# Optimization experiments

Measured on AMD Instinct MI355X. Metric: run time of the kernel, lower is better.

Reference implementation:

```python
import jax, jax.numpy as jnp
import numpy as np

FEATURE_DIM = 128
NUM_EDGES = 640000
NUM_NODES = 40000


def setup_inputs() -> dict:
    key = jax.random.key(0)
    ks = jax.random.split(key, 10)
    d = FEATURE_DIM
    scale = 1.0 / np.sqrt(d)
    inp = {
        "messages": jax.random.normal(ks[0], (NUM_EDGES, d), dtype=jnp.float32),
        "receivers": jax.random.randint(ks[1], (NUM_EDGES,), 0, NUM_NODES, dtype=jnp.int32),
        "num_segments": NUM_NODES,
        "Wk": jax.random.normal(ks[2], (d, d), dtype=jnp.float32) * scale,
        "bk": jnp.zeros((d,), dtype=jnp.float32),
        "Wv": jax.random.normal(ks[3], (d, d), dtype=jnp.float32) * scale,
        "bv": jnp.zeros((d,), dtype=jnp.float32),
        "Wq": jax.random.normal(ks[4], (d, d), dtype=jnp.float32) * scale,
        "bq": jnp.zeros((d,), dtype=jnp.float32),
        "Wo": jax.random.normal(ks[5], (d, d), dtype=jnp.float32) * scale,
        "bo": jnp.zeros((d,), dtype=jnp.float32),
    }
    return inp


def reference(messages, receivers, num_segments, Wk, bk, Wv, bv, Wq, bq, Wo, bo):
    d = messages.shape[-1]
    # per-edge key/value projections
    keys = messages @ Wk + bk            # [E, d]
    values = messages @ Wv + bv          # [E, d]
    # node-level summed messages -> queries
    summed = jax.ops.segment_sum(messages, receivers, num_segments)  # [N, d]
    queries = summed @ Wq + bq                                       # [N, d]
    # scalar attention score per edge (dot over full feature dim)
    msg_q = queries[receivers]                                       # [E, d]
    scores = jnp.sum(msg_q * keys, axis=-1) / jnp.sqrt(jnp.float32(d))  # [E]
    # segment softmax over edges sharing a receiver
    max_s = jax.ops.segment_max(scores, receivers, num_segments)     # [N]
    exp_s = jnp.exp(scores - max_s[receivers])                       # [E]
    sum_e = jax.ops.segment_sum(exp_s, receivers, num_segments)      # [N]
    attn = exp_s / (sum_e[receivers] + 1e-08)                        # [E]
    # weighted scatter-sum of values, then output projection
    agg = jax.ops.segment_sum(values * attn[:, None], receivers, num_segments)  # [N, d]
    return agg @ Wo + bo
```

## Files before the change

kernel.cpp:

```cpp
#include <hip/hip_runtime.h>

#define D 128
#define RSQRT_D 0.088388347648318440550f
#define NEG_HUGE -3.4e38f
#define NPB 8
#define CAP 288
#define DTHR 20.0f

#define FMA4(acc, s, b) { acc.x += (s)*(b).x; acc.y += (s)*(b).y; acc.z += (s)*(b).z; acc.w += (s)*(b).w; }
#define ADD4(acc, b) { acc.x += (b).x; acc.y += (b).y; acc.z += (b).z; acc.w += (b).w; }
#define MRG4(a) { a.x += __shfl_xor(a.x,32); a.y += __shfl_xor(a.y,32); a.z += __shfl_xor(a.z,32); a.w += __shfl_xor(a.w,32); }
#define SCL4(a, f) { a.x *= (f); a.y *= (f); a.z *= (f); a.w *= (f); }
#define Z4 make_float4(0.f,0.f,0.f,0.f)

#define MERGE_HALVES(mi, si, ci) { \
    float mo_ = __shfl_xor(mi, 32); \
    float so_ = __shfl_xor(si, 32); \
    float4 co_; co_.x = __shfl_xor(ci.x, 32); co_.y = __shfl_xor(ci.y, 32); \
    co_.z = __shfl_xor(ci.z, 32); co_.w = __shfl_xor(ci.w, 32); \
    float mt_ = fmaxf(mi, mo_); \
    float e0_ = __expf(mi - mt_), e1_ = __expf(mo_ - mt_); \
    si = si * e0_ + so_ * e1_; \
    ci.x = ci.x * e0_ + co_.x * e1_; ci.y = ci.y * e0_ + co_.y * e1_; \
    ci.z = ci.z * e0_ + co_.z * e1_; ci.w = ci.w * e0_ + co_.w * e1_; \
}

__global__ __launch_bounds__(256) void prep_kernel(
    const float* __restrict__ Wq, const float* __restrict__ Wk,
    const float* __restrict__ bq, const float* __restrict__ bk,
    const float* __restrict__ Wv, const float* __restrict__ Wo,
    const float* __restrict__ bv,
    float* __restrict__ Wqk, float* __restrict__ bqk,
    float* __restrict__ wqb, float* __restrict__ bqb,
    float* __restrict__ Wvo, float* __restrict__ bvo,
    int* __restrict__ zbase, int zcount) {
    int bid = blockIdx.x, t = threadIdx.x;
    if (bid < 64) {
        int i = bid * 2 + (t >> 7), j = t & 127;
        float a1 = 0.f, a2 = 0.f;
        for (int u = 0; u < D; ++u) {
            a1 += Wq[i * D + u] * Wk[j * D + u];
            a2 += Wv[i * D + u] * Wo[u * D + j];
        }
        Wqk[i * D + j] = a1;
        Wvo[i * D + j] = a2;
    } else if (bid == 64) {
        if (t < D) {
            int j = t;
            float a1 = 0.f, a2 = 0.f, a3 = 0.f;
            for (int u = 0; u < D; ++u) {
                a1 += bq[u] * Wk[j * D + u];
                a2 += Wq[j * D + u] * bk[u];
                a3 += bv[u] * Wo[u * D + j];
            }
            bqk[j] = a1; wqb[j] = a2; bvo[j] = a3;
            if (j == 0) {
                float b = 0.f;
                for (int u = 0; u < D; ++u) b += bq[u] * bk[u];
                *bqb = b;
            }
        }
    } else {
        int idx = (bid - 65) * 256 + t;
        if (idx < zcount) zbase[idx] = 0;
    }
}

__global__ void hist_kernel(const int* __restrict__ recv, int* __restrict__ cnt, int E) {
    int i = blockIdx.x * blockDim.x + threadIdx.x;
    int base = i << 2;
    if (base + 3 < E) {
        int4 r = *(const int4*)(recv + base);
        atomicAdd(&cnt[r.x], 1);
        atomicAdd(&cnt[r.y], 1);
        atomicAdd(&cnt[r.z], 1);
        atomicAdd(&cnt[r.w], 1);
    } else {
        for (int u = base; u < E; ++u) atomicAdd(&cnt[recv[u]], 1);
    }
}

__global__ __launch_bounds__(1024) void scan_kernel(const int* __restrict__ cnt,
                                                    int* __restrict__ start, int N) {
    __shared__ int wsum[16];
    __shared__ int chunk_total;
    int t = threadIdx.x;
    int w = t >> 6, lane = t & 63;
    int running = 0;
    const int4* cnt4 = (const int4*)cnt;
    int nIter = (N + 4095) >> 12;
    int4 v = make_int4(0, 0, 0, 0);
    {
        int i = t << 2;
        if (i < N) v = cnt4[i >> 2];
    }
    for (int it = 0; it < nIter; ++it) {
        int4 vn = make_int4(0, 0, 0, 0);
        {
            int i = ((it + 1) << 12) + (t << 2);
            if (it + 1 < nIter && i < N) vn = cnt4[i >> 2];
        }
        int s0 = v.x, s1 = s0 + v.y, s2 = s1 + v.z, s3 = s2 + v.w;
        int x = s3;
#pragma unroll
        for (int off = 1; off < 64; off <<= 1) {
            int y = __shfl_up(x, off);
            if (lane >= off) x += y;
        }
        if (lane == 63) wsum[w] = x;
        __syncthreads();
        if (w == 0 && lane < 16) {
            int s = wsum[lane];
#pragma unroll
            for (int off = 1; off < 16; off <<= 1) {
                int y = __shfl_up(s, off);
                if (lane >= off) s += y;
            }
            wsum[lane] = s;
            if (lane == 15) chunk_total = s;
        }
        __syncthreads();
        int waveoff = (w == 0) ? 0 : wsum[w - 1];
        int tb = running + waveoff + (x - s3);
        int i = (it << 12) + (t << 2);
        if (i < N) ((int4*)start)[i >> 2] = make_int4(tb, tb + s0, tb + s1, tb + s2);
        running += chunk_total;
        __syncthreads();
        v = vn;
    }
    if (t == 0) start[N] = running;
}

__global__ void fill_kernel(const int* __restrict__ recv, const int* __restrict__ start,
                            int* __restrict__ cursor, int* __restrict__ eidx, int E) {
    int e = blockIdx.x * blockDim.x + threadIdx.x;
    if (e >= E) return;
    int r = recv[e];
    int p = atomicAdd(&cursor[r], 1);
    eidx[start[r] + p] = e;
}

__device__ __forceinline__ float hdot32(float4 f, float4 q) {
    float p = f.x * q.x + f.y * q.y + f.z * q.z + f.w * q.w;
    p += __shfl_xor(p, 1); p += __shfl_xor(p, 2); p += __shfl_xor(p, 4);
    p += __shfl_xor(p, 8); p += __shfl_xor(p, 16);
    return p;
}

__global__ __launch_bounds__(128, 4) void mega_kernel(
    const float* __restrict__ msg, const int* __restrict__ eidx,
    const int* __restrict__ start,
    const float* __restrict__ Wqk, const float* __restrict__ bqk,
    const float* __restrict__ wqb, const float* __restrict__ bqbp,
    const float* __restrict__ Wvo, const float* __restrict__ bvo,
    const float* __restrict__ bo,
    float* __restrict__ out, int N) {
    __shared__ float4 sums4[NPB * 32];
    __shared__ float4 qks4[NPB * 32];
    __shared__ int eidx_s[CAP];
    __shared__ float sat[NPB];

    int t = threadIdx.x;
    int lane = t & 63, w = t >> 6;
    int h = lane >> 5;
    int k = lane & 31;
    int base = blockIdx.x * NPB;
    const float4* msg4 = (const float4*)msg;

    int nendB = min(base + NPB, N);
    int s0B = start[base];
    int cntB = start[nendB] - s0B;
    int cc = min(cntB, CAP);
    for (int i = t; i < cc; i += 128) eidx_s[i] = eidx[s0B + i];

    int n0 = base + w * 4;
    int b0 = start[min(n0 + 0, N)] - s0B;
    int b1 = start[min(n0 + 1, N)] - s0B;
    int b2 = start[min(n0 + 2, N)] - s0B;
    int b3 = start[min(n0 + 3, N)] - s0B;
    int b4 = start[min(n0 + 4, N)] - s0B;

    __syncthreads();

    auto loadrow = [&](int r) -> float4 {
        int rI = min(r, b4 - 1);
        int e = (rI < CAP) ? eidx_s[rI] : eidx[s0B + rI];
        return msg4[(size_t)e * 32 + k];
    };

    float4 a0 = Z4, a1 = Z4, a2 = Z4, a3 = Z4;
    if (b0 < b4) {
        int j = b0;
        float4 F0 = loadrow(j + h), F1 = loadrow(j + h + 2),
               F2 = loadrow(j + h + 4), F3 = loadrow(j + h + 6);
        for (;;) {
            int jn = j + 8;
            bool more = jn < b4;
            float4 G0, G1, G2, G3;
            if (more) {
                G0 = loadrow(jn + h); G1 = loadrow(jn + h + 2);
                G2 = loadrow(jn + h + 4); G3 = loadrow(jn + h + 6);
            }
#pragma unroll
            for (int u = 0; u < 4; ++u) {
                int r = j + h + 2 * u;
                float4 g = (u == 0) ? F0 : (u == 1) ? F1 : (u == 2) ? F2 : F3;
                float mk = (r < b4) ? 1.f : 0.f;
                g.x *= mk; g.y *= mk; g.z *= mk; g.w *= mk;
                if (r < b1)      { ADD4(a0, g); }
                else if (r < b2) { ADD4(a1, g); }
                else if (r < b3) { ADD4(a2, g); }
                else             { ADD4(a3, g); }
            }
            if (!more) break;
            F0 = G0; F1 = G1; F2 = G2; F3 = G3;
            j = jn;
        }
    }
    MRG4(a0); MRG4(a1); MRG4(a2); MRG4(a3);
    if (lane < 32) {
        sums4[(w * 4 + 0) * 32 + k] = a0;
        sums4[(w * 4 + 1) * 32 + k] = a1;
        sums4[(w * 4 + 2) * 32 + k] = a2;
        sums4[(w * 4 + 3) * 32 + k] = a3;
    }
    __syncthreads();

    {
        int c = t & 31, slot = t >> 5;
        const float4* B4 = (const float4*)Wqk;
        float4 acc0 = ((const float4*)bqk)[c];
        float4 acc1 = acc0;
        for (int i = 0; i < D; i += 4) {
            float4 aA = sums4[slot * 32 + (i >> 2)];
            float4 aB = sums4[(slot + 4) * 32 + (i >> 2)];
            float4 c0 = B4[(i + 0) * 32 + c];
            float4 c1 = B4[(i + 1) * 32 + c];
            float4 c2 = B4[(i + 2) * 32 + c];
            float4 c3 = B4[(i + 3) * 32 + c];
            FMA4(acc0, aA.x, c0); FMA4(acc0, aA.y, c1); FMA4(acc0, aA.z, c2); FMA4(acc0, aA.w, c3);
            FMA4(acc1, aB.x, c0); FMA4(acc1, aB.y, c1); FMA4(acc1, aB.z, c2); FMA4(acc1, aB.w, c3);
        }
        qks4[slot * 32 + c] = acc0;
        qks4[(slot + 4) * 32 + c] = acc1;
    }
    __syncthreads();

    {
        float4 wv = ((const float4*)wqb)[k];
        float bqb = bqbp[0];
        float4 sv0 = sums4[(w * 4 + 0) * 32 + k];
        float4 sv1 = sums4[(w * 4 + 1) * 32 + k];
        float4 sv2 = sums4[(w * 4 + 2) * 32 + k];
        float4 sv3 = sums4[(w * 4 + 3) * 32 + k];
        float qb0 = hdot32(sv0, wv) + bqb;
        float qb1 = hdot32(sv1, wv) + bqb;
        float qb2 = hdot32(sv2, wv) + bqb;
        float qb3 = hdot32(sv3, wv) + bqb;
        float4 q0 = qks4[(w * 4 + 0) * 32 + k];
        float4 q1 = qks4[(w * 4 + 1) * 32 + k];
        float4 q2 = qks4[(w * 4 + 2) * 32 + k];
        float4 q3 = qks4[(w * 4 + 3) * 32 + k];

        float m0 = NEG_HUGE, m1 = NEG_HUGE, m2 = NEG_HUGE, m3 = NEG_HUGE;
        float sm0 = 0.f, sm1 = 0.f, sm2 = 0.f, sm3 = 0.f;
        float4 c0 = Z4, c1 = Z4, c2 = Z4, c3 = Z4;
        if (b0 < b4) {
            int j = b0;
            float4 F0 = loadrow(j + h), F1 = loadrow(j + h + 2),
                   F2 = loadrow(j + h + 4), F3 = loadrow(j + h + 6);
            for (;;) {
                int jn = j + 8;
                bool more = jn < b4;
                float4 G0, G1, G2, G3;
                if (more) {
                    G0 = loadrow(jn + h); G1 = loadrow(jn + h + 2);
                    G2 = loadrow(jn + h + 4); G3 = loadrow(jn + h + 6);
                }
#pragma unroll
                for (int u = 0; u < 4; ++u) {
                    int r = j + h + 2 * u;
                    bool valid = r < b4;
                    float4 f = (u == 0) ? F0 : (u == 1) ? F1 : (u == 2) ? F2 : F3;
                    float4 qv = (r < b1) ? q0 : (r < b2) ? q1 : (r < b3) ? q2 : q3;
                    float qbv = (r < b1) ? qb0 : (r < b2) ? qb1 : (r < b3) ? qb2 : qb3;
                    float sc = (hdot32(f, qv) + qbv) * RSQRT_D;
                    float msel = (r < b1) ? m0 : (r < b2) ? m1 : (r < b3) ? m2 : m3;
                    if (valid && sc > msel + DTHR) {
                        float fac = __expf(msel - sc);
                        if (r < b1)      { sm0 *= fac; SCL4(c0, fac); m0 = sc; }
                        else if (r < b2) { sm1 *= fac; SCL4(c1, fac); m1 = sc; }
                        else if (r < b3) { sm2 *= fac; SCL4(c2, fac); m2 = sc; }
                        else             { sm3 *= fac; SCL4(c3, fac); m3 = sc; }
                        msel = sc;
                    }
                    float wgt = valid ? __expf(sc - msel) : 0.f;
                    if (r < b1)      { sm0 += wgt; FMA4(c0, wgt, f); }
                    else if (r < b2) { sm1 += wgt; FMA4(c1, wgt, f); }
                    else if (r < b3) { sm2 += wgt; FMA4(c2, wgt, f); }
                    else             { sm3 += wgt; FMA4(c3, wgt, f); }
                }
                if (!more) break;
                F0 = G0; F1 = G1; F2 = G2; F3 = G3;
                j = jn;
            }
        }
        MERGE_HALVES(m0, sm0, c0);
        MERGE_HALVES(m1, sm1, c1);
        MERGE_HALVES(m2, sm2, c2);
        MERGE_HALVES(m3, sm3, c3);
        float inv0 = 1.f / (sm0 + 1e-8f);
        float inv1 = 1.f / (sm1 + 1e-8f);
        float inv2 = 1.f / (sm2 + 1e-8f);
        float inv3 = 1.f / (sm3 + 1e-8f);
        if (lane < 32) {
            sums4[(w * 4 + 0) * 32 + k] = make_float4(c0.x * inv0, c0.y * inv0, c0.z * inv0, c0.w * inv0);
            sums4[(w * 4 + 1) * 32 + k] = make_float4(c1.x * inv1, c1.y * inv1, c1.z * inv1, c1.w * inv1);
            sums4[(w * 4 + 2) * 32 + k] = make_float4(c2.x * inv2, c2.y * inv2, c2.z * inv2, c2.w * inv2);
            sums4[(w * 4 + 3) * 32 + k] = make_float4(c3.x * inv3, c3.y * inv3, c3.z * inv3, c3.w * inv3);
        }
        if (lane == 0) {
            sat[w * 4 + 0] = sm0 * inv0;
            sat[w * 4 + 1] = sm1 * inv1;
            sat[w * 4 + 2] = sm2 * inv2;
            sat[w * 4 + 3] = sm3 * inv3;
        }
    }
    __syncthreads();

    {
        int c = t & 31, slot = t >> 5;
        const float4* B4 = (const float4*)Wvo;
        float4 bo4 = ((const float4*)bo)[c];
        float4 bv4 = ((const float4*)bvo)[c];
        float sa0 = sat[slot], sa1 = sat[slot + 4];
        float4 acc0 = make_float4(bo4.x + sa0 * bv4.x, bo4.y + sa0 * bv4.y,
                                  bo4.z + sa0 * bv4.z, bo4.w + sa0 * bv4.w);
        float4 acc1 = make_float4(bo4.x + sa1 * bv4.x, bo4.y + sa1 * bv4.y,
                                  bo4.z + sa1 * bv4.z, bo4.w + sa1 * bv4.w);
        for (int i = 0; i < D; i += 4) {
            float4 aA = sums4[slot * 32 + (i >> 2)];
            float4 aB = sums4[(slot + 4) * 32 + (i >> 2)];
            float4 d0 = B4[(i + 0) * 32 + c];
            float4 d1 = B4[(i + 1) * 32 + c];
            float4 d2 = B4[(i + 2) * 32 + c];
            float4 d3 = B4[(i + 3) * 32 + c];
            FMA4(acc0, aA.x, d0); FMA4(acc0, aA.y, d1); FMA4(acc0, aA.z, d2); FMA4(acc0, aA.w, d3);
            FMA4(acc1, aB.x, d0); FMA4(acc1, aB.y, d1); FMA4(acc1, aB.z, d2); FMA4(acc1, aB.w, d3);
        }
        int nA = base + slot, nB = base + slot + 4;
        if (nA < N) ((float4*)(out + (size_t)nA * D))[c] = acc0;
        if (nB < N) ((float4*)(out + (size_t)nB * D))[c] = acc1;
    }
}


extern "C" void kernel_launch(void* const* d_in, const int* in_sizes, int n_in,
                              void* d_out, int out_size, void* d_ws, size_t ws_size,
                              hipStream_t stream) {
    const float* msg = (const float*)d_in[0];
    const int* recv = (const int*)d_in[1];
    const float* Wk = (const float*)d_in[3];
    const float* bk = (const float*)d_in[4];
    const float* Wv = (const float*)d_in[5];
    const float* bv = (const float*)d_in[6];
    const float* Wq = (const float*)d_in[7];
    const float* bq = (const float*)d_in[8];
    const float* Wo = (const float*)d_in[9];
    const float* bo = (const float*)d_in[10];
    float* out = (float*)d_out;

    int E = in_sizes[0] / D;
    int N = out_size / D;

    char* wsb = (char*)d_ws;
    size_t o = 0;
    auto alloc = [&](size_t elems) {
        void* p = wsb + o;
        o += (elems * 4 + 63) & ~(size_t)63;
        return p;
    };

    int* cnt    = (int*)alloc(2 * (size_t)N);
    int* cursor = cnt + N;
    int* start  = (int*)alloc(N + 1);
    int* eidx   = (int*)alloc(E);
    float* Wqk  = (float*)alloc(D * D);
    float* bqk  = (float*)alloc(D);
    float* wqb  = (float*)alloc(D);
    float* bqb  = (float*)alloc(1);
    float* Wvo  = (float*)alloc(D * D);
    float* bvo  = (float*)alloc(D);

    int zcount = 2 * N;
    int zblocks = (zcount + 255) / 256;
    prep_kernel<<<65 + zblocks, 256, 0, stream>>>(Wq, Wk, bq, bk, Wv, Wo, bv,
                                                  Wqk, bqk, wqb, bqb, Wvo, bvo,
                                                  cnt, zcount);
    int E4 = (E + 3) / 4;
    int nbE4 = (E4 + 255) / 256;
    hist_kernel<<<nbE4, 256, 0, stream>>>(recv, cnt, E);
    scan_kernel<<<1, 1024, 0, stream>>>(cnt, start, N);
    int nbE = (E + 255) / 256;
    fill_kernel<<<nbE, 256, 0, stream>>>(recv, start, cursor, eidx, E);
    mega_kernel<<<(N + NPB - 1) / NPB, 128, 0, stream>>>(msg, eidx, start, Wqk, bqk, wqb, bqb,
                                                         Wvo, bvo, bo, out, N);
}
```

Measured before the change: 667.6 us.

## Make each wavefront own two nodes and replace block barriers with LDS waits

The mega kernel is restructured so each 64-lane wavefront processes two nodes independently, with per-wave shared buffers, instead of a 128-thread block sharing eight nodes. Block-wide __syncthreads are replaced by s_waitcnt lgkmcnt(0) fences, which is enough because each wave only touches its own LDS slice. This cuts barrier stalls and load imbalance between waves, and doubles the grid size. In exchange the per-node dense projections no longer share Wqk/Wvo loads across four node slots, so weight traffic per node goes up, and the per-wave eidx cache shrinks to 96 entries.

```diff
diff --git a/kernel.cpp b/kernel.cpp
--- a/kernel.cpp
+++ b/kernel.cpp
@@ -3,8 +3,8 @@
 #define D 128
 #define RSQRT_D 0.088388347648318440550f
 #define NEG_HUGE -3.4e38f
-#define NPB 8
-#define CAP 288
+#define NPT 2
+#define CAPW 96
 #define DTHR 20.0f
 
 #define FMA4(acc, s, b) { acc.x += (s)*(b).x; acc.y += (s)*(b).y; acc.z += (s)*(b).z; acc.w += (s)*(b).w; }
@@ -12,6 +12,8 @@
 #define MRG4(a) { a.x += __shfl_xor(a.x,32); a.y += __shfl_xor(a.y,32); a.z += __shfl_xor(a.z,32); a.w += __shfl_xor(a.w,32); }
 #define SCL4(a, f) { a.x *= (f); a.y *= (f); a.z *= (f); a.w *= (f); }
 #define Z4 make_float4(0.f,0.f,0.f,0.f)
+
+#define LDS_FENCE() asm volatile("s_waitcnt lgkmcnt(0)" ::: "memory")
 
 #define MERGE_HALVES(mi, si, ci) { \
     float mo_ = __shfl_xor(mi, 32); \
@@ -155,47 +157,41 @@
     const float* __restrict__ Wvo, const float* __restrict__ bvo,
     const float* __restrict__ bo,
     float* __restrict__ out, int N) {
-    __shared__ float4 sums4[NPB * 32];
-    __shared__ float4 qks4[NPB * 32];
-    __shared__ int eidx_s[CAP];
-    __shared__ float sat[NPB];
+    __shared__ float4 sums4[2][NPT * 32];
+    __shared__ float4 qks4[2][NPT * 32];
+    __shared__ int    eidx_s[2][CAPW];
+    __shared__ float  sat[2][NPT];
 
     int t = threadIdx.x;
     int lane = t & 63, w = t >> 6;
     int h = lane >> 5;
     int k = lane & 31;
-    int base = blockIdx.x * NPB;
     const float4* msg4 = (const float4*)msg;
 
-    int nendB = min(base + NPB, N);
-    int s0B = start[base];
-    int cntB = start[nendB] - s0B;
-    int cc = min(cntB, CAP);
-    for (int i = t; i < cc; i += 128) eidx_s[i] = eidx[s0B + i];
-
-    int n0 = base + w * 4;
-    int b0 = start[min(n0 + 0, N)] - s0B;
-    int b1 = start[min(n0 + 1, N)] - s0B;
-    int b2 = start[min(n0 + 2, N)] - s0B;
-    int b3 = start[min(n0 + 3, N)] - s0B;
-    int b4 = start[min(n0 + 4, N)] - s0B;
-
-    __syncthreads();
+    int n0 = (blockIdx.x * 2 + w) * NPT;
+    if (n0 >= N) return;
+    int s0W = start[n0];
+    int b1 = start[min(n0 + 1, N)] - s0W;
+    int b2 = start[min(n0 + 2, N)] - s0W;
+
+    int cc = min(b2, CAPW);
+    for (int i = lane; i < cc; i += 64) eidx_s[w][i] = eidx[s0W + i];
+    LDS_FENCE();
 
     auto loadrow = [&](int r) -> float4 {
-        int rI = min(r, b4 - 1);
-        int e = (rI < CAP) ? eidx_s[rI] : eidx[s0B + rI];
+        int rI = min(r, b2 - 1);
+        int e = (rI < CAPW) ? eidx_s[w][rI] : eidx[s0W + rI];
         return msg4[(size_t)e * 32 + k];
     };
 
-    float4 a0 = Z4, a1 = Z4, a2 = Z4, a3 = Z4;
-    if (b0 < b4) {
-        int j = b0;
-        float4 F0 = loadrow(j + h), F1 = loadrow(j + h + 2),
-               F2 = loadrow(j + h + 4), F3 = loadrow(j + h + 6);
+    float4 a0 = Z4, a1 = Z4;
+    if (b2 > 0) {
+        int j = 0;
+        float4 F0 = loadrow(h), F1 = loadrow(h + 2),
+               F2 = loadrow(h + 4), F3 = loadrow(h + 6);
         for (;;) {
             int jn = j + 8;
-            bool more = jn < b4;
+            bool more = jn < b2;
             float4 G0, G1, G2, G3;
             if (more) {
                 G0 = loadrow(jn + h); G1 = loadrow(jn + h + 2);
@@ -204,74 +200,60 @@
 #pragma unroll
             for (int u = 0; u < 4; ++u) {
                 int r = j + h + 2 * u;
-                float4 g = (u == 0) ? F0 : (u == 1) ? F1 : (u == 2) ? F2 : F3;
-                float mk = (r < b4) ? 1.f : 0.f;
-                g.x *= mk; g.y *= mk; g.z *= mk; g.w *= mk;
-                if (r < b1)      { ADD4(a0, g); }
-                else if (r < b2) { ADD4(a1, g); }
-                else if (r < b3) { ADD4(a2, g); }
-                else             { ADD4(a3, g); }
+                float4 gq = (u == 0) ? F0 : (u == 1) ? F1 : (u == 2) ? F2 : F3;
+                float mk = (r < b2) ? 1.f : 0.f;
+                gq.x *= mk; gq.y *= mk; gq.z *= mk; gq.w *= mk;
+                if (r < b1) { ADD4(a0, gq); }
+                else        { ADD4(a1, gq); }
             }
             if (!more) break;
             F0 = G0; F1 = G1; F2 = G2; F3 = G3;
             j = jn;
         }
     }
-    MRG4(a0); MRG4(a1); MRG4(a2); MRG4(a3);
+    MRG4(a0); MRG4(a1);
     if (lane < 32) {
-        sums4[(w * 4 + 0) * 32 + k] = a0;
-        sums4[(w * 4 + 1) * 32 + k] = a1;
-        sums4[(w * 4 + 2) * 32 + k] = a2;
-        sums4[(w * 4 + 3) * 32 + k] = a3;
-    }
-    __syncthreads();
+        sums4[w][0 * 32 + k] = a0;
+        sums4[w][1 * 32 + k] = a1;
+    }
+    LDS_FENCE();
 
     {
-        int c = t & 31, slot = t >> 5;
+        int c = k, slot = h;
         const float4* B4 = (const float4*)Wqk;
         float4 acc0 = ((const float4*)bqk)[c];
-        float4 acc1 = acc0;
         for (int i = 0; i < D; i += 4) {
-            float4 aA = sums4[slot * 32 + (i >> 2)];
-            float4 aB = sums4[(slot + 4) * 32 + (i >> 2)];
-            float4 c0 = B4[(i + 0) * 32 + c];
-            float4 c1 = B4[(i + 1) * 32 + c];
-            float4 c2 = B4[(i + 2) * 32 + c];
-            float4 c3 = B4[(i + 3) * 32 + c];
-            FMA4(acc0, aA.x, c0); FMA4(acc0, aA.y, c1); FMA4(acc0, aA.z, c2); FMA4(acc0, aA.w, c3);
-            FMA4(acc1, aB.x, c0); FMA4(acc1, aB.y, c1); FMA4(acc1, aB.z, c2); FMA4(acc1, aB.w, c3);
-        }
-        qks4[slot * 32 + c] = acc0;
-        qks4[(slot + 4) * 32 + c] = acc1;
-    }
-    __syncthreads();
+            float4 aA = sums4[w][slot * 32 + (i >> 2)];
+            float4 d0 = B4[(i + 0) * 32 + c];
+            float4 d1 = B4[(i + 1) * 32 + c];
+            float4 d2 = B4[(i + 2) * 32 + c];
+            float4 d3 = B4[(i + 3) * 32 + c];
+            FMA4(acc0, aA.x, d0); FMA4(acc0, aA.y, d1); FMA4(acc0, aA.z, d2); FMA4(acc0, aA.w, d3);
+        }
+        qks4[w][slot * 32 + c] = acc0;
+    }
+    LDS_FENCE();
 
     {
         float4 wv = ((const float4*)wqb)[k];
         float bqb = bqbp[0];
-        float4 sv0 = sums4[(w * 4 + 0) * 32 + k];
-        float4 sv1 = sums4[(w * 4 + 1) * 32 + k];
-        float4 sv2 = sums4[(w * 4 + 2) * 32 + k];
-        float4 sv3 = sums4[(w * 4 + 3) * 32 + k];
+        float4 sv0 = sums4[w][0 * 32 + k];
+        float4 sv1 = sums4[w][1 * 32 + k];
         float qb0 = hdot32(sv0, wv) + bqb;
         float qb1 = hdot32(sv1, wv) + bqb;
-        float qb2 = hdot32(sv2, wv) + bqb;
-        float qb3 = hdot32(sv3, wv) + bqb;
-        float4 q0 = qks4[(w * 4 + 0) * 32 + k];
-        float4 q1 = qks4[(w * 4 + 1) * 32 + k];
-        float4 q2 = qks4[(w * 4 + 2) * 32 + k];
-        float4 q3 = qks4[(w * 4 + 3) * 32 + k];
-
-        float m0 = NEG_HUGE, m1 = NEG_HUGE, m2 = NEG_HUGE, m3 = NEG_HUGE;
-        float sm0 = 0.f, sm1 = 0.f, sm2 = 0.f, sm3 = 0.f;
-        float4 c0 = Z4, c1 = Z4, c2 = Z4, c3 = Z4;
-        if (b0 < b4) {
-            int j = b0;
-            float4 F0 = loadrow(j + h), F1 = loadrow(j + h + 2),
-                   F2 = loadrow(j + h + 4), F3 = loadrow(j + h + 6);
+        float4 q0 = qks4[w][0 * 32 + k];
+        float4 q1 = qks4[w][1 * 32 + k];
+
+        float m0 = NEG_HUGE, m1 = NEG_HUGE;
+        float sm0 = 0.f, sm1 = 0.f;
+        float4 c0 = Z4, c1 = Z4;
+        if (b2 > 0) {
+            int j = 0;
+            float4 F0 = loadrow(h), F1 = loadrow(h + 2),
+                   F2 = loadrow(h + 4), F3 = loadrow(h + 6);
             for (;;) {
                 int jn = j + 8;
-                bool more = jn < b4;
+                bool more = jn < b2;
                 float4 G0, G1, G2, G3;
                 if (more) {
                     G0 = loadrow(jn + h); G1 = loadrow(jn + h + 2);
@@ -280,25 +262,22 @@
 #pragma unroll
                 for (int u = 0; u < 4; ++u) {
                     int r = j + h + 2 * u;
-                    bool valid = r < b4;
+                    bool valid = r < b2;
                     float4 f = (u == 0) ? F0 : (u == 1) ? F1 : (u == 2) ? F2 : F3;
-                    float4 qv = (r < b1) ? q0 : (r < b2) ? q1 : (r < b3) ? q2 : q3;
-                    float qbv = (r < b1) ? qb0 : (r < b2) ? qb1 : (r < b3) ? qb2 : qb3;
+                    bool first = r < b1;
+                    float4 qv = first ? q0 : q1;
+                    float qbv = first ? qb0 : qb1;
                     float sc = (hdot32(f, qv) + qbv) * RSQRT_D;
-                    float msel = (r < b1) ? m0 : (r < b2) ? m1 : (r < b3) ? m2 : m3;
+                    float msel = first ? m0 : m1;
                     if (valid && sc > msel + DTHR) {
                         float fac = __expf(msel - sc);
-                        if (r < b1)      { sm0 *= fac; SCL4(c0, fac); m0 = sc; }
-                        else if (r < b2) { sm1 *= fac; SCL4(c1, fac); m1 = sc; }
-                        else if (r < b3) { sm2 *= fac; SCL4(c2, fac); m2 = sc; }
-                        else             { sm3 *= fac; SCL4(c3, fac); m3 = sc; }
+                        if (first) { sm0 *= fac; SCL4(c0, fac); m0 = sc; }
+                        else       { sm1 *= fac; SCL4(c1, fac); m1 = sc; }
                         msel = sc;
                     }
                     float wgt = valid ? __expf(sc - msel) : 0.f;
-                    if (r < b1)      { sm0 += wgt; FMA4(c0, wgt, f); }
-                    else if (r < b2) { sm1 += wgt; FMA4(c1, wgt, f); }
-                    else if (r < b3) { sm2 += wgt; FMA4(c2, wgt, f); }
-                    else             { sm3 += wgt; FMA4(c3, wgt, f); }
+                    if (first) { sm0 += wgt; FMA4(c0, wgt, f); }
+                    else       { sm1 += wgt; FMA4(c1, wgt, f); }
                 }
                 if (!more) break;
                 F0 = G0; F1 = G1; F2 = G2; F3 = G3;
@@ -307,50 +286,37 @@
         }
         MERGE_HALVES(m0, sm0, c0);
         MERGE_HALVES(m1, sm1, c1);
-        MERGE_HALVES(m2, sm2, c2);
-        MERGE_HALVES(m3, sm3, c3);
         float inv0 = 1.f / (sm0 + 1e-8f);
         float inv1 = 1.f / (sm1 + 1e-8f);
-        float inv2 = 1.f / (sm2 + 1e-8f);
-        float inv3 = 1.f / (sm3 + 1e-8f);
         if (lane < 32) {
-            sums4[(w * 4 + 0) * 32 + k] = make_float4(c0.x * inv0, c0.y * inv0, c0.z * inv0, c0.w * inv0);
-            sums4[(w * 4 + 1) * 32 + k] = make_float4(c1.x * inv1, c1.y * inv1, c1.z * inv1, c1.w * inv1);
-            sums4[(w * 4 + 2) * 32 + k] = make_float4(c2.x * inv2, c2.y * inv2, c2.z * inv2, c2.w * inv2);
-            sums4[(w * 4 + 3) * 32 + k] = make_float4(c3.x * inv3, c3.y * inv3, c3.z * inv3, c3.w * inv3);
+            sums4[w][0 * 32 + k] = make_float4(c0.x * inv0, c0.y * inv0, c0.z * inv0, c0.w * inv0);
+            sums4[w][1 * 32 + k] = make_float4(c1.x * inv1, c1.y * inv1, c1.z * inv1, c1.w * inv1);
         }
         if (lane == 0) {
-            sat[w * 4 + 0] = sm0 * inv0;
-            sat[w * 4 + 1] = sm1 * inv1;
-            sat[w * 4 + 2] = sm2 * inv2;
-            sat[w * 4 + 3] = sm3 * inv3;
-        }
-    }
-    __syncthreads();
+            sat[w][0] = sm0 * inv0;
+            sat[w][1] = sm1 * inv1;
+        }
+    }
+    LDS_FENCE();
 
     {
-        int c = t & 31, slot = t >> 5;
+        int c = k, slot = h;
         const float4* B4 = (const float4*)Wvo;
         float4 bo4 = ((const float4*)bo)[c];
         float4 bv4 = ((const float4*)bvo)[c];
-        float sa0 = sat[slot], sa1 = sat[slot + 4];
-        float4 acc0 = make_float4(bo4.x + sa0 * bv4.x, bo4.y + sa0 * bv4.y,
-                                  bo4.z + sa0 * bv4.z, bo4.w + sa0 * bv4.w);
-        float4 acc1 = make_float4(bo4.x + sa1 * bv4.x, bo4.y + sa1 * bv4.y,
-                                  bo4.z + sa1 * bv4.z, bo4.w + sa1 * bv4.w);
+        float sa = sat[w][slot];
+        float4 acc0 = make_float4(bo4.x + sa * bv4.x, bo4.y + sa * bv4.y,
+                                  bo4.z + sa * bv4.z, bo4.w + sa * bv4.w);
         for (int i = 0; i < D; i += 4) {
-            float4 aA = sums4[slot * 32 + (i >> 2)];
-            float4 aB = sums4[(slot + 4) * 32 + (i >> 2)];
+            float4 aA = sums4[w][slot * 32 + (i >> 2)];
             float4 d0 = B4[(i + 0) * 32 + c];
             float4 d1 = B4[(i + 1) * 32 + c];
             float4 d2 = B4[(i + 2) * 32 + c];
             float4 d3 = B4[(i + 3) * 32 + c];
             FMA4(acc0, aA.x, d0); FMA4(acc0, aA.y, d1); FMA4(acc0, aA.z, d2); FMA4(acc0, aA.w, d3);
-            FMA4(acc1, aB.x, d0); FMA4(acc1, aB.y, d1); FMA4(acc1, aB.z, d2); FMA4(acc1, aB.w, d3);
-        }
-        int nA = base + slot, nB = base + slot + 4;
+        }
+        int nA = n0 + slot;
         if (nA < N) ((float4*)(out + (size_t)nA * D))[c] = acc0;
-        if (nB < N) ((float4*)(out + (size_t)nB * D))[c] = acc1;
     }
 }
 
@@ -403,6 +369,7 @@
     scan_kernel<<<1, 1024, 0, stream>>>(cnt, start, N);
     int nbE = (E + 255) / 256;
     fill_kernel<<<nbE, 256, 0, stream>>>(recv, start, cursor, eidx, E);
-    mega_kernel<<<(N + NPB - 1) / NPB, 128, 0, stream>>>(msg, eidx, start, Wqk, bqk, wqb, bqb,
-                                                         Wvo, bvo, bo, out, N);
-}
+    int nblk = (N + 2 * NPT - 1) / (2 * NPT);
+    mega_kernel<<<nblk, 128, 0, stream>>>(msg, eidx, start, Wqk, bqk, wqb, bqb,
+                                          Wvo, bvo, bo, out, N);
+}
```

Measured after the change: 688.0 us. 3.1% more time.
